# Kernel tuning notes

Measured on AMD Instinct MI355X. Metric: run time of the kernel, lower is better.

Reference implementation:

```python
import jax, jax.numpy as jnp
import numpy as np

B, F, A, U = 4096, 64, 8, 32  # batch, n_features, num_att, n_outputs
R = 2.0                       # the 'r' scaling inside exp(kernel * r)


def setup_inputs() -> dict:
    key = jax.random.key(0)
    k1, k2 = jax.random.split(key)
    inputs = jax.random.normal(k1, (B, F), dtype=jnp.float32)
    # per-exclusion-feature attention kernels, stacked: [F, A, F, U]
    limit = float(np.sqrt(6.0 / (F + U)))  # glorot_uniform
    kernels = jax.random.uniform(k2, (F, A, F, U), dtype=jnp.float32,
                                 minval=-limit, maxval=limit)
    return {"inputs": inputs, "kernels": kernels}


def reference(inputs, kernels):
    # inputs: [B, F]; kernels: [j=F excluded-feature index, A, F, U]
    f = inputs.shape[-1]
    mask = 1.0 - jnp.eye(f, dtype=inputs.dtype)          # [j, F]: zero out feature j
    xm = mask[:, None, :] * inputs[None, :, :]           # [j, B, F]
    z = jnp.einsum('jbf,jafu->jabu', xm, kernels)        # [j, A, B, U]
    z = jax.nn.softmax(z, axis=-1)                       # softmax over units
    w = jnp.exp(kernels * R)                             # [j, A, F, U]
    scores = jnp.einsum('jabu,jafu->jabf', z, w)         # [j, A, B, F]
    scores = scores.mean(axis=0)                         # mean over exclusion axis -> [A, B, F]
    return jax.nn.softmax(scores, axis=-1)               # [A, B, F]
```

## Files before the change

### kernel.cpp

```cpp
#include <hip/hip_runtime.h>
#include <hip/hip_bf16.h>
#include <math.h>

#define B_ 4096
#define F_ 64
#define A_ 8
#define U_ 32

typedef float f32x4 __attribute__((ext_vector_type(4)));
typedef short bf16x8 __attribute__((ext_vector_type(8)));

#define KD_OFF (4ull << 20)

static __device__ __forceinline__ unsigned int pk_bf16(float lo, float hi) {
    union { __hip_bfloat162 h2; unsigned int u; } cv;
    cv.h2 = __float22bfloat162_rn(make_float2(lo, hi));
    return cv.u;
}
static __device__ __forceinline__ float rb(float f) {
    unsigned int u = __float_as_uint(f);
    u += 0x7FFFu + ((u >> 16) & 1u);
    return __uint_as_float(u & 0xFFFF0000u);
}

__global__ __launch_bounds__(256) void ife_prep(const float* __restrict__ kern,
                                                unsigned char* __restrict__ ws)
{
    const int bid = blockIdx.x;
    const int a = bid >> 6, j = bid & 63;
    const int t = threadIdx.x;
    __shared__ float st[64][36];

    const float* src = kern + ((size_t)j * A_ + a) * (F_ * U_);
    {
        const int f = t >> 2, u0 = (t & 3) * 8;
        *(float4*)&st[f][u0]     = *(const float4*)&src[f * U_ + u0];
        *(float4*)&st[f][u0 + 4] = *(const float4*)&src[f * U_ + u0 + 4];
    }
    __syncthreads();

    unsigned char* dst = ws + (size_t)bid * 8192;
    const int fragid = t >> 6, lane = t & 63, q = lane >> 4, c = lane & 15;

    {
        const int kc = fragid >> 1, ut = fragid & 1;
        const int f0 = kc * 32 + q * 8, u = ut * 16 + c;
        unsigned int w[4];
        #pragma unroll
        for (int i = 0; i < 4; ++i)
            w[i] = pk_bf16(st[f0 + 2 * i][u], st[f0 + 2 * i + 1][u]);
        *(uint4*)(dst + fragid * 1024 + lane * 16) = make_uint4(w[0], w[1], w[2], w[3]);
    }
    {
        const int f = fragid * 16 + c, u0 = q * 8;
        const float4 wa = *(const float4*)&st[f][u0];
        const float4 wb = *(const float4*)&st[f][u0 + 4];
        unsigned int w[4];
        w[0] = pk_bf16(__expf(2.f * wa.x), __expf(2.f * wa.y));
        w[1] = pk_bf16(__expf(2.f * wa.z), __expf(2.f * wa.w));
        w[2] = pk_bf16(__expf(2.f * wb.x), __expf(2.f * wb.y));
        w[3] = pk_bf16(__expf(2.f * wb.z), __expf(2.f * wb.w));
        *(uint4*)(dst + 4096 + fragid * 1024 + lane * 16) = make_uint4(w[0], w[1], w[2], w[3]);
    }
    if (t < U_)
        ((float*)(ws + KD_OFF))[(size_t)bid * U_ + t] = rb(st[j][t]);
}

__global__ __launch_bounds__(256, 2) void ife_main(const float* __restrict__ x,
                                                   const unsigned char* __restrict__ ws,
                                                   float* __restrict__ out)
{
    const int a = blockIdx.y, bt = blockIdx.x, t = threadIdx.x;
    const int wv = t >> 6, lane = t & 63, q = lane >> 4, c = lane & 15;

    __shared__ float Xf[64][66];
    __shared__ float Kd[64][32];
    __shared__ __align__(16) unsigned int Pbuf[4][16][20];

    bf16x8 Xh[2];
    {
        const float* xr = x + (size_t)(bt * 64 + wv * 16 + c) * F_;
        #pragma unroll
        for (int kc = 0; kc < 2; ++kc) {
            const float4 va = *(const float4*)&xr[kc * 32 + q * 8];
            const float4 vb = *(const float4*)&xr[kc * 32 + q * 8 + 4];
            union { unsigned int u[4]; bf16x8 v; } H;
            H.u[0] = pk_bf16(va.x, va.y);
            H.u[1] = pk_bf16(va.z, va.w);
            H.u[2] = pk_bf16(vb.x, vb.y);
            H.u[3] = pk_bf16(vb.z, vb.w);
            Xh[kc] = H.v;
        }
    }
    {
        const int row = t >> 2, cb = (t & 3) * 16;
        const float* xsrc = x + (size_t)(bt * 64 + row) * F_ + cb;
        #pragma unroll
        for (int i = 0; i < 16; i += 4) {
            const float4 v = *(const float4*)&xsrc[i];
            Xf[row][cb + i]     = rb(v.x);
            Xf[row][cb + i + 1] = rb(v.y);
            Xf[row][cb + i + 2] = rb(v.z);
            Xf[row][cb + i + 3] = rb(v.w);
        }
    }
    {
        const float* kd = (const float*)(ws + KD_OFF) + (size_t)a * 64 * U_;
        const int jj = t >> 2, u0 = (t & 3) * 8;
        *(float4*)&Kd[jj][u0]     = *(const float4*)&kd[jj * U_ + u0];
        *(float4*)&Kd[jj][u0 + 4] = *(const float4*)&kd[jj * U_ + u0 + 4];
    }
    __syncthreads();

    const unsigned int psel = (q < 2) ? 0x05040100u : 0x07060302u;
    const unsigned char* fbase = ws + (size_t)a * 64 * 8192 + (size_t)lane * 16;

    union { unsigned int u[4]; bf16x8 v; } oc;
    oc.u[0] = 0x3F803F80u; oc.u[1] = 0x3F803F80u; oc.u[2] = 0x3F803F80u; oc.u[3] = 0x3F803F80u;
    const bf16x8 ONES = oc.v;
    const f32x4 vzero = (f32x4){0.f, 0.f, 0.f, 0.f};

    f32x4 S0 = vzero, S1 = vzero, S2 = vzero, S3 = vzero;

    bf16x8 KA[4], WA[4], KB[4], WB[4];

    auto LOADF = [&](bf16x8* K, bf16x8* W, int jj) {
        const unsigned char* p = fbase + (size_t)jj * 8192;
        #pragma unroll
        for (int i = 0; i < 4; ++i) {
            K[i] = *(const bf16x8*)(p + i * 1024);
            W[i] = *(const bf16x8*)(p + 4096 + i * 1024);
        }
    };

    auto BODY = [&](const bf16x8* K, const bf16x8* W, int j) {
        f32x4 ZA = vzero, ZB = vzero;
        ZA = __builtin_amdgcn_mfma_f32_16x16x32_bf16(Xh[0], K[0], ZA, 0, 0, 0);
        ZA = __builtin_amdgcn_mfma_f32_16x16x32_bf16(Xh[1], K[2], ZA, 0, 0, 0);
        ZB = __builtin_amdgcn_mfma_f32_16x16x32_bf16(Xh[0], K[1], ZB, 0, 0, 0);
        ZB = __builtin_amdgcn_mfma_f32_16x16x32_bf16(Xh[1], K[3], ZB, 0, 0, 0);

        const float kd0 = Kd[j][c], kd1 = Kd[j][16 + c];
        #pragma unroll
        for (int r = 0; r < 4; ++r) {
            const float xj = Xf[wv * 16 + q * 4 + r][j];
            const float e0 = __expf(ZA[r] - xj * kd0);
            const float e1 = __expf(ZB[r] - xj * kd1);
            Pbuf[wv][q * 4 + r][c] = pk_bf16(e0, e1);
        }
        asm volatile("s_waitcnt lgkmcnt(0)" ::: "memory");
        union { unsigned int u[4]; bf16x8 v; } E;
        {
            const uint4 pa = *(const uint4*)&Pbuf[wv][c][(q & 1) * 8];
            const uint4 pb = *(const uint4*)&Pbuf[wv][c][(q & 1) * 8 + 4];
            E.u[0] = __builtin_amdgcn_perm(pa.y, pa.x, psel);
            E.u[1] = __builtin_amdgcn_perm(pa.w, pa.z, psel);
            E.u[2] = __builtin_amdgcn_perm(pb.y, pb.x, psel);
            E.u[3] = __builtin_amdgcn_perm(pb.w, pb.z, psel);
        }

        const f32x4 sv = __builtin_amdgcn_mfma_f32_16x16x32_bf16(E.v, ONES, vzero, 0, 0, 0);
        f32x4 D0 = __builtin_amdgcn_mfma_f32_16x16x32_bf16(E.v, W[0], vzero, 0, 0, 0);
        f32x4 D1 = __builtin_amdgcn_mfma_f32_16x16x32_bf16(E.v, W[1], vzero, 0, 0, 0);
        f32x4 D2 = __builtin_amdgcn_mfma_f32_16x16x32_bf16(E.v, W[2], vzero, 0, 0, 0);
        f32x4 D3 = __builtin_amdgcn_mfma_f32_16x16x32_bf16(E.v, W[3], vzero, 0, 0, 0);
        #pragma unroll
        for (int r = 0; r < 4; ++r) {
            const float inv = __builtin_amdgcn_rcpf(sv[r]);
            S0[r] += D0[r] * inv;
            S1[r] += D1[r] * inv;
            S2[r] += D2[r] * inv;
            S3[r] += D3[r] * inv;
        }
    };

    LOADF(KA, WA, 0);
    for (int j = 0; j < 64; j += 2) {
        LOADF(KB, WB, j + 1);
        BODY(KA, WA, j);
        LOADF(KA, WA, (j + 2 < 64) ? (j + 2) : 63);
        BODY(KB, WB, j + 1);
    }

    const float sc = 1.f / 64.f;
    #pragma unroll
    for (int r = 0; r < 4; ++r) {
        const float e0 = __expf(S0[r] * sc);
        const float e1 = __expf(S1[r] * sc);
        const float e2 = __expf(S2[r] * sc);
        const float e3 = __expf(S3[r] * sc);
        float s = e0 + e1 + e2 + e3;
        s += __shfl_xor(s, 1);
        s += __shfl_xor(s, 2);
        s += __shfl_xor(s, 4);
        s += __shfl_xor(s, 8);
        const float inv = 1.f / s;
        const int b = bt * 64 + wv * 16 + q * 4 + r;
        float* o = out + ((size_t)a * B_ + b) * F_ + c;
        o[0]  = e0 * inv;
        o[16] = e1 * inv;
        o[32] = e2 * inv;
        o[48] = e3 * inv;
    }
}

extern "C" void kernel_launch(void* const* d_in, const int* in_sizes, int n_in,
                              void* d_out, int out_size, void* d_ws, size_t ws_size,
                              hipStream_t stream) {
    (void)in_sizes; (void)n_in; (void)out_size; (void)ws_size;
    const float* x    = (const float*)d_in[0];
    const float* kern = (const float*)d_in[1];
    float* out        = (float*)d_out;
    unsigned char* ws = (unsigned char*)d_ws;

    hipLaunchKernelGGL(ife_prep, dim3(F_ * A_), dim3(256), 0, stream, kern, ws);
    hipLaunchKernelGGL(ife_main, dim3(B_ / 64, A_), dim3(256), 0, stream, x, ws, out);
}
```

Baseline: 98.67 us.

## Software-pipeline the softmax stage across exclusion iterations with double-buffered LDS

Splits the per-j body into a scores/exp stage that writes to shared memory and a read-plus-weighted-sum stage. With two LDS buffers, the exp stage for the next j runs while the previous buffer is read. The scalar Xf/Kd loads are also hoisted one iteration ahead. The explicit lgkmcnt wait is replaced by a compiler barrier. The aim is to hide LDS round-trip latency and keep the MFMA and VALU work overlapped, at the cost of more registers and LDS, which may hurt occupancy under launch_bounds(256,2).

```diff
diff --git a/kernel.cpp b/kernel.cpp
--- a/kernel.cpp
+++ b/kernel.cpp
@@ -75,7 +75,8 @@
 
     __shared__ float Xf[64][66];
     __shared__ float Kd[64][32];
-    __shared__ __align__(16) unsigned int Pbuf[4][16][20];
+    __shared__ __align__(16) unsigned int PbufA[4][16][20];
+    __shared__ __align__(16) unsigned int PbufB[4][16][20];
 
     bf16x8 Xh[2];
     {
@@ -123,6 +124,8 @@
     f32x4 S0 = vzero, S1 = vzero, S2 = vzero, S3 = vzero;
 
     bf16x8 KA[4], WA[4], KB[4], WB[4];
+    float xjA[4], xjB[4], kdA0, kdA1, kdB0, kdB1;
+    uint4 ra0, ra1, rb0, rb1;
 
     auto LOADF = [&](bf16x8* K, bf16x8* W, int jj) {
         const unsigned char* p = fbase + (size_t)jj * 8192;
@@ -133,31 +136,40 @@
         }
     };
 
-    auto BODY = [&](const bf16x8* K, const bf16x8* W, int j) {
+    auto SCAL = [&](float* xj, float& k0, float& k1, int j) {
+        #pragma unroll
+        for (int r = 0; r < 4; ++r) xj[r] = Xf[wv * 16 + q * 4 + r][j];
+        k0 = Kd[j][c];
+        k1 = Kd[j][16 + c];
+    };
+
+    auto ZW = [&](const bf16x8* K, const float* xj, float kd0, float kd1,
+                  unsigned int (*P)[16][20]) {
         f32x4 ZA = vzero, ZB = vzero;
         ZA = __builtin_amdgcn_mfma_f32_16x16x32_bf16(Xh[0], K[0], ZA, 0, 0, 0);
         ZA = __builtin_amdgcn_mfma_f32_16x16x32_bf16(Xh[1], K[2], ZA, 0, 0, 0);
         ZB = __builtin_amdgcn_mfma_f32_16x16x32_bf16(Xh[0], K[1], ZB, 0, 0, 0);
         ZB = __builtin_amdgcn_mfma_f32_16x16x32_bf16(Xh[1], K[3], ZB, 0, 0, 0);
-
-        const float kd0 = Kd[j][c], kd1 = Kd[j][16 + c];
         #pragma unroll
         for (int r = 0; r < 4; ++r) {
-            const float xj = Xf[wv * 16 + q * 4 + r][j];
-            const float e0 = __expf(ZA[r] - xj * kd0);
-            const float e1 = __expf(ZB[r] - xj * kd1);
-            Pbuf[wv][q * 4 + r][c] = pk_bf16(e0, e1);
-        }
-        asm volatile("s_waitcnt lgkmcnt(0)" ::: "memory");
+            const float e0 = __expf(ZA[r] - xj[r] * kd0);
+            const float e1 = __expf(ZB[r] - xj[r] * kd1);
+            P[wv][q * 4 + r][c] = pk_bf16(e0, e1);
+        }
+    };
+
+    auto RD = [&](uint4& pa, uint4& pb, const unsigned int (*P)[16][20]) {
+        asm volatile("" ::: "memory");
+        pa = *(const uint4*)&P[wv][c][(q & 1) * 8];
+        pb = *(const uint4*)&P[wv][c][(q & 1) * 8 + 4];
+    };
+
+    auto FN = [&](const uint4& pa, const uint4& pb, const bf16x8* W) {
         union { unsigned int u[4]; bf16x8 v; } E;
-        {
-            const uint4 pa = *(const uint4*)&Pbuf[wv][c][(q & 1) * 8];
-            const uint4 pb = *(const uint4*)&Pbuf[wv][c][(q & 1) * 8 + 4];
-            E.u[0] = __builtin_amdgcn_perm(pa.y, pa.x, psel);
-            E.u[1] = __builtin_amdgcn_perm(pa.w, pa.z, psel);
-            E.u[2] = __builtin_amdgcn_perm(pb.y, pb.x, psel);
-            E.u[3] = __builtin_amdgcn_perm(pb.w, pb.z, psel);
-        }
+        E.u[0] = __builtin_amdgcn_perm(pa.y, pa.x, psel);
+        E.u[1] = __builtin_amdgcn_perm(pa.w, pa.z, psel);
+        E.u[2] = __builtin_amdgcn_perm(pb.y, pb.x, psel);
+        E.u[3] = __builtin_amdgcn_perm(pb.w, pb.z, psel);
 
         const f32x4 sv = __builtin_amdgcn_mfma_f32_16x16x32_bf16(E.v, ONES, vzero, 0, 0, 0);
         f32x4 D0 = __builtin_amdgcn_mfma_f32_16x16x32_bf16(E.v, W[0], vzero, 0, 0, 0);
@@ -175,12 +187,28 @@
     };
 
     LOADF(KA, WA, 0);
-    for (int j = 0; j < 64; j += 2) {
-        LOADF(KB, WB, j + 1);
-        BODY(KA, WA, j);
-        LOADF(KA, WA, (j + 2 < 64) ? (j + 2) : 63);
-        BODY(KB, WB, j + 1);
-    }
+    SCAL(xjA, kdA0, kdA1, 0);
+    ZW(KA, xjA, kdA0, kdA1, PbufA);
+    LOADF(KB, WB, 1);
+    SCAL(xjB, kdB0, kdB1, 1);
+
+    for (int j = 0; j < 62; j += 2) {
+        RD(ra0, ra1, PbufA);
+        ZW(KB, xjB, kdB0, kdB1, PbufB);
+        FN(ra0, ra1, WA);
+        LOADF(KA, WA, j + 2);
+        SCAL(xjA, kdA0, kdA1, j + 2);
+        RD(rb0, rb1, PbufB);
+        ZW(KA, xjA, kdA0, kdA1, PbufA);
+        FN(rb0, rb1, WB);
+        LOADF(KB, WB, j + 3);
+        SCAL(xjB, kdB0, kdB1, j + 3);
+    }
+    RD(ra0, ra1, PbufA);
+    ZW(KB, xjB, kdB0, kdB1, PbufB);
+    FN(ra0, ra1, WA);
+    RD(rb0, rb1, PbufB);
+    FN(rb0, rb1, WB);
 
     const float sc = 1.f / 64.f;
     #pragma unroll
```

Result: no change. 97.35 us (-1.3%).
